# Kernel tuning notes

Hardware: AMD Instinct MI355X
Metric: run time of the kernel (lower is better)

## Reference

```python
import jax, jax.numpy as jnp
import numpy as np

DIM = 256
NUM_HEADS = 8
HEAD_DIM = DIM // NUM_HEADS


def setup_inputs() -> dict:
    key = jax.random.key(0)
    k_x, k_wq, k_bq, k_wp, k_bp = jax.random.split(key, 5)
    x = jax.random.normal(k_x, (4, DIM, 64, 64), dtype=jnp.float32)
    # 1x1 convs == per-pixel linear layers over channels
    w_qkv = jax.random.normal(k_wq, (3 * DIM, DIM), dtype=jnp.float32) * (DIM ** -0.5)
    b_qkv = jax.random.normal(k_bq, (3 * DIM,), dtype=jnp.float32) * 0.02
    w_proj = jax.random.normal(k_wp, (DIM, DIM), dtype=jnp.float32) * (DIM ** -0.5)
    b_proj = jax.random.normal(k_bp, (DIM,), dtype=jnp.float32) * 0.02
    return {"x": x, "w_qkv": w_qkv, "b_qkv": b_qkv, "w_proj": w_proj, "b_proj": b_proj}


def reference(x, w_qkv, b_qkv, w_proj, b_proj):
    B, C, H, W = x.shape
    S = H * W
    h, d = NUM_HEADS, HEAD_DIM
    # flatten spatial dims: (B, C, H, W) -> (B, S, C)
    xf = x.reshape(B, C, S).transpose(0, 2, 1)
    # 1x1 conv qkv: (B, S, 3C)
    qkv = xf @ w_qkv.T + b_qkv
    q, k, v = jnp.split(qkv, 3, axis=-1)
    # channel dim splits as (heads, head_dim): (B, S, C) -> (B, h, S, d)
    split = lambda t: t.reshape(B, S, h, d).transpose(0, 2, 1, 3)
    q, k, v = split(q), split(k), split(v)
    scale = d ** -0.5
    attn = jnp.einsum('bhsd,bhtd->bhst', q, k) * scale  # (B, h, S, S)
    attn = jax.nn.softmax(attn, axis=-1)
    out = jnp.einsum('bhst,bhtd->bhsd', attn, v)
    # merge heads: (B, h, S, d) -> (B, S, C)
    out = out.transpose(0, 2, 1, 3).reshape(B, S, C)
    out = out @ w_proj.T + b_proj
    # back to (B, C, H, W)
    return out.transpose(0, 2, 1).reshape(B, C, H, W)
```

## Files before the change

### kernel.cpp

```cpp
#include <hip/hip_runtime.h>


typedef __attribute__((ext_vector_type(8))) short short8;
typedef __attribute__((ext_vector_type(4))) float f4;

__device__ __forceinline__ short f2bs(float f) {
  union { float f; unsigned u; } v; v.f = f;
  unsigned r = v.u + 0x7FFFu + ((v.u >> 16) & 1u);
  return (short)(r >> 16);
}

__device__ __forceinline__ int pkrne(float a, float b) {
  return (int)((unsigned short)f2bs(a) | ((unsigned)f2bs(b) << 16));
}

__device__ __forceinline__ int pkhu(float lo, float hi) {
  union { float f; unsigned u; } a, b; a.f = lo; b.f = hi;
  return (int)__builtin_amdgcn_perm(b.u + 0x8000u, a.u + 0x8000u, 0x07060302u);
}

__global__ __launch_bounds__(256) void k_prep_w(
    const float* __restrict__ wq, const float* __restrict__ wp,
    short* __restrict__ wqb, short* __restrict__ wpb) {
  const int i = blockIdx.x * 256 + threadIdx.x;
  const int NQ = 768 * 256 / 4;
  f4 v; short* dst; int off;
  if (i < NQ) { v = ((const f4*)wq)[i]; dst = wqb; off = i * 4; }
  else        { v = ((const f4*)wp)[i - NQ]; dst = wpb; off = (i - NQ) * 4; }
  int2 pr; pr.x = pkrne(v[0], v[1]); pr.y = pkrne(v[2], v[3]);
  *(int2*)(dst + off) = pr;
}

__global__ __launch_bounds__(256) void k_prep_x(
    const float* __restrict__ x, short* __restrict__ xT) {
  const int t = threadIdx.x;
  const int b = blockIdx.z, c0 = blockIdx.y * 64, s0 = blockIdx.x * 64;
  __shared__ __align__(16) short tile[64 * 64];
#pragma unroll
  for (int pass = 0; pass < 4; ++pass) {
    const int cl = pass * 16 + (t >> 4);
    const int sl = (t & 15) * 4;
    f4 v = *(const f4*)(x + ((size_t)(b * 256 + c0 + cl)) * 4096 + s0 + sl);
#pragma unroll
    for (int k = 0; k < 4; ++k) {
      const int s = sl + k;
      tile[s * 64 + (cl ^ ((s & 7) << 3))] = f2bs(v[k]);
    }
  }
  __syncthreads();
#pragma unroll
  for (int i = 0; i < 2; ++i) {
    const int s = t >> 2;
    const int gc = (t & 3) + i * 4;
    const int gg = gc ^ (s & 7);
    short8 row = *(const short8*)(tile + s * 64 + gg * 8);
    *(short8*)(xT + ((size_t)(b * 4096 + s0 + s)) * 256 + c0 + gc * 8) = row;
  }
}

__global__ __launch_bounds__(256) void k_qkv(
    const short* __restrict__ xT, const short* __restrict__ wqb,
    const float* __restrict__ bias,
    short* __restrict__ Qr, short* __restrict__ Kq, short* __restrict__ Vt) {
  const int tid = threadIdx.x;
  const int L = tid & 63, wv = tid >> 6;
  const int ln15 = L & 15, quad = L >> 4;
  const int mt = blockIdx.x;
  const int b = mt >> 6;
  const int s0 = (mt & 63) << 6;
  const int j0 = blockIdx.y << 6;
  const int jw = j0 + wv * 16;

  __shared__ __align__(16) short tl[4][1024];

  f4 acc[4] = {{0,0,0,0},{0,0,0,0},{0,0,0,0},{0,0,0,0}};
  const short* wb = wqb + (jw + ln15) * 256 + quad * 8;
  const short* xb = xT + (size_t)(b * 4096 + s0 + ln15) * 256 + quad * 8;

#pragma unroll
  for (int cb = 0; cb < 256; cb += 32) {
    short8 af = *(const short8*)(wb + cb);
#pragma unroll
    for (int sub = 0; sub < 4; ++sub) {
      short8 bfr = *(const short8*)(xb + sub * (16 * 256) + cb);
      acc[sub] = __builtin_amdgcn_mfma_f32_16x16x32_bf16(af, bfr, acc[sub], 0, 0, 0);
    }
  }
  float bj[4];
#pragma unroll
  for (int r = 0; r < 4; ++r) bj[r] = bias[jw + quad * 4 + r];

  const int type = j0 >> 8;
  const int hj = jw & 255;
  const int bh = b * 8 + (hj >> 5);
  const int db = hj & 31;

  if (type != 2) {
    const float qsc = 0.17677669529663689f * 1.44269504088896f;
    const float mul = (type == 0) ? qsc : 1.0f;
    short* dst = (type == 0) ? Qr : Kq;
#pragma unroll
    for (int sub = 0; sub < 4; ++sub) {
      float v0 = (acc[sub][0] + bj[0]) * mul;
      float v1 = (acc[sub][1] + bj[1]) * mul;
      float v2 = (acc[sub][2] + bj[2]) * mul;
      float v3 = (acc[sub][3] + bj[3]) * mul;
      int2 pr; pr.x = pkhu(v0, v1); pr.y = pkhu(v2, v3);
      *(int2*)(dst + (size_t)(bh * 4096 + s0 + sub * 16 + ln15) * 32 + db + quad * 4) = pr;
    }
  } else {
    short* tv = tl[wv];
#pragma unroll
    for (int sub = 0; sub < 4; ++sub) {
      const int s = sub * 16 + ln15;
#pragma unroll
      for (int r = 0; r < 4; ++r) {
        const int dl = quad * 4 + r;
        tv[dl * 64 + ((((s >> 3) ^ dl) & 7) << 3) + (s & 7)] = f2bs(acc[sub][r] + bj[r]);
      }
    }
#pragma unroll
    for (int i = 0; i < 2; ++i) {
      const int dl = i * 8 + (L >> 3);
      const int gs = L & 7;
      const int gg = gs ^ (dl & 7);
      short8 row = *(const short8*)(tv + dl * 64 + gg * 8);
      *(short8*)(Vt + (size_t)(bh * 32 + db + dl) * 4096 + s0 + gs * 8) = row;
    }
  }
}

__global__ __launch_bounds__(256, 6) void k_attn(
    const short* __restrict__ Qr, const short* __restrict__ Kq,
    const short* __restrict__ Vt, short* __restrict__ O) {
  const int tid = threadIdx.x;
  const int L = tid & 63, wv = tid >> 6;
  const int ln15 = L & 15, quad = L >> 4;
  const int bh = blockIdx.y;
  const int b = bh >> 3, h = bh & 7;
  const int qt = wv & 1, half = wv >> 1;
  const int qb = blockIdx.x * 64 + qt * 32;

  const short* Qb = Qr + (size_t)bh * 4096 * 32;
  const short* Kb = Kq + (size_t)bh * 4096 * 32 + half * 2048 * 32;
  const short* Vb = Vt + (size_t)bh * 32 * 4096 + half * 2048;

  __shared__ __align__(16) short plds[4][2048];
  __shared__ float l_up[2][32];
  short* pw = plds[wv];
  const int sw = ln15 & 14;

  short8 qf[2];
#pragma unroll
  for (int qs = 0; qs < 2; ++qs)
    qf[qs] = *(const short8*)(Qb + (qb + qs * 16 + ln15) * 32 + quad * 8);

  f4 acc[2][2] = {{{0,0,0,0},{0,0,0,0}},{{0,0,0,0},{0,0,0,0}}};
  float lsum[2] = {0.f, 0.f};
  const f4 z4 = {0.f, 0.f, 0.f, 0.f};

  const short* kp = Kb + ln15 * 32 + quad * 8;
  const short* vp = Vb + ln15 * 4096 + quad * 8;

  for (int kb = 0; kb < 2048; kb += 64) {
#pragma unroll
    for (int t = 0; t < 4; ++t) {
      short8 kf = *(const short8*)(kp + (kb + t * 16) * 32);
#pragma unroll
      for (int qs = 0; qs < 2; ++qs) {
        f4 sc = __builtin_amdgcn_mfma_f32_16x16x32_bf16(kf, qf[qs], z4, 0, 0, 0);
        float p0 = __builtin_amdgcn_exp2f(sc[0]);
        float p1 = __builtin_amdgcn_exp2f(sc[1]);
        float p2 = __builtin_amdgcn_exp2f(sc[2]);
        float p3 = __builtin_amdgcn_exp2f(sc[3]);
        lsum[qs] += (p0 + p1) + (p2 + p3);
        int2 pr;
        pr.x = pkhu(p0, p1);
        pr.y = pkhu(p2, p3);
        const int gw = ((t << 2) + quad) ^ sw;
        *(int2*)(pw + qs * 1024 + ln15 * 64 + gw * 4) = pr;
      }
    }
#pragma unroll
    for (int ks = 0; ks < 2; ++ks) {
      short8 vf0 = *(const short8*)(vp + kb + ks * 32);
      short8 vf1 = *(const short8*)(vp + 16 * 4096 + kb + ks * 32);
#pragma unroll
      for (int qs = 0; qs < 2; ++qs) {
        const int g0 = ((ks << 3) + (quad << 1)) ^ sw;
        short8 pf = *(const short8*)(pw + qs * 1024 + ln15 * 64 + g0 * 4);
        acc[qs][0] = __builtin_amdgcn_mfma_f32_16x16x32_bf16(pf, vf0, acc[qs][0], 0, 0, 0);
        acc[qs][1] = __builtin_amdgcn_mfma_f32_16x16x32_bf16(pf, vf1, acc[qs][1], 0, 0, 0);
      }
    }
  }

  float lfull[2];
#pragma unroll
  for (int qs = 0; qs < 2; ++qs) {
    float l = lsum[qs];
    l += __shfl_xor(l, 16);
    l += __shfl_xor(l, 32);
    lfull[qs] = l;
  }

  if (half == 1) {
    float* cw = (float*)plds[wv];
#pragma unroll
    for (int qs = 0; qs < 2; ++qs) {
#pragma unroll
      for (int dg = 0; dg < 2; ++dg)
#pragma unroll
        for (int r = 0; r < 4; ++r)
          cw[(qs * 16 + quad * 4 + r) * 32 + dg * 16 + ln15] = acc[qs][dg][r];
      if (quad == 0) l_up[qt][qs * 16 + ln15] = lfull[qs];
    }
  }
  __syncthreads();
  if (half == 0) {
    const float* cu = (const float*)plds[wv + 2];
#pragma unroll
    for (int qs = 0; qs < 2; ++qs) {
#pragma unroll
      for (int r = 0; r < 4; ++r) {
        const float lown = __shfl(lfull[qs], quad * 4 + r);
        const float lup = l_up[qt][qs * 16 + quad * 4 + r];
        const float rl = 1.0f / (lown + lup);
        const int sg = qb + qs * 16 + quad * 4 + r;
        short* op = O + (size_t)(b * 4096 + sg) * 256 + h * 32 + ln15;
        const int ci = (qs * 16 + quad * 4 + r) * 32 + ln15;
        op[0]  = f2bs((acc[qs][0][r] + cu[ci]) * rl);
        op[16] = f2bs((acc[qs][1][r] + cu[ci + 16]) * rl);
      }
    }
  }
}

__global__ __launch_bounds__(256) void k_proj(
    const short* __restrict__ O, const short* __restrict__ wpb,
    const float* __restrict__ bias, float* __restrict__ out) {
  const int tid = threadIdx.x;
  const int L = tid & 63, wv = tid >> 6;
  const int ln15 = L & 15, quad = L >> 4;
  const int m0 = blockIdx.x * 64 + wv * 16;
  const int n0 = blockIdx.y << 6;
  const int b = m0 >> 12, s0 = m0 & 4095;

  f4 acc[4] = {{0,0,0,0},{0,0,0,0},{0,0,0,0},{0,0,0,0}};
  const short* Ob = O + (size_t)(m0 + ln15) * 256 + quad * 8;
  const short* wb = wpb + (n0 + ln15) * 256 + quad * 8;

#pragma unroll
  for (int cb = 0; cb < 256; cb += 32) {
    short8 af = *(const short8*)(Ob + cb);
#pragma unroll
    for (int sub = 0; sub < 4; ++sub) {
      short8 bfr = *(const short8*)(wb + sub * (16 * 256) + cb);
      acc[sub] = __builtin_amdgcn_mfma_f32_16x16x32_bf16(af, bfr, acc[sub], 0, 0, 0);
    }
  }
#pragma unroll
  for (int sub = 0; sub < 4; ++sub) {
    const int c = n0 + sub * 16 + ln15;
    const float bv = bias[c];
    f4 v;
#pragma unroll
    for (int r = 0; r < 4; ++r) v[r] = acc[sub][r] + bv;
    *(f4*)(out + (size_t)b * (256 * 4096) + (size_t)c * 4096 + s0 + quad * 4) = v;
  }
}

extern "C" void kernel_launch(void* const* d_in, const int* in_sizes, int n_in,
                              void* d_out, int out_size, void* d_ws, size_t ws_size,
                              hipStream_t stream) {
  const float* x      = (const float*)d_in[0];
  const float* w_qkv  = (const float*)d_in[1];
  const float* b_qkv  = (const float*)d_in[2];
  const float* w_proj = (const float*)d_in[3];
  const float* b_proj = (const float*)d_in[4];
  float* out = (float*)d_out;

  const size_t SEG = (size_t)4 * 8 * 4096 * 32;
  short* Qr  = (short*)d_ws;
  short* Kq  = Qr + SEG;
  short* Vt  = Kq + SEG;
  short* OX  = Vt + SEG;
  short* wqb = OX + SEG;
  short* wpb = wqb + 768 * 256;

  k_prep_w<<<256, 256, 0, stream>>>(w_qkv, w_proj, wqb, wpb);
  k_prep_x<<<dim3(64, 4, 4), 256, 0, stream>>>(x, OX);
  k_qkv <<<dim3(256, 12), 256, 0, stream>>>(OX, wqb, b_qkv, Qr, Kq, Vt);
  k_attn<<<dim3(64, 32),  256, 0, stream>>>(Qr, Kq, Vt, OX);
  k_proj<<<dim3(256, 4),  256, 0, stream>>>(OX, wpb, b_proj, out);
}
```

Baseline: 366.3 us.

## Switch attention to 32x32x16 MFMA with register-resident P and permuted V layout

Rewrites the attention inner loop around 32x32x16 bf16 MFMAs. The score accumulator layout now matches the B-operand layout of the PV product, so exponentiated probabilities are packed straight into registers and no longer round-trip through LDS. The QKV kernel writes V in a permuted column order so each lane's V fragment lines up with that register layout. The intent is to drop the per-tile LDS writes and reads of P and to issue fewer, larger MFMAs. In exchange, the 16-float accumulators raise register pressure, and the occupancy hint in launch bounds is removed.

```diff
diff --git a/kernel.cpp b/kernel.cpp
--- a/kernel.cpp
+++ b/kernel.cpp
@@ -3,6 +3,7 @@
 
 typedef __attribute__((ext_vector_type(8))) short short8;
 typedef __attribute__((ext_vector_type(4))) float f4;
+typedef __attribute__((ext_vector_type(16))) float f16v;
 
 __device__ __forceinline__ short f2bs(float f) {
   union { float f; unsigned u; } v; v.f = f;
@@ -17,6 +18,11 @@
 __device__ __forceinline__ int pkhu(float lo, float hi) {
   union { float f; unsigned u; } a, b; a.f = lo; b.f = hi;
   return (int)__builtin_amdgcn_perm(b.u + 0x8000u, a.u + 0x8000u, 0x07060302u);
+}
+
+__device__ __forceinline__ short8 mk8(int a, int b, int c, int d) {
+  int4 t; t.x = a; t.y = b; t.z = c; t.w = d;
+  short8 r; __builtin_memcpy(&r, &t, 16); return r;
 }
 
 __global__ __launch_bounds__(256) void k_prep_w(
@@ -61,7 +67,7 @@
 __global__ __launch_bounds__(256) void k_qkv(
     const short* __restrict__ xT, const short* __restrict__ wqb,
     const float* __restrict__ bias,
-    short* __restrict__ Qr, short* __restrict__ Kq, short* __restrict__ Vt) {
+    short* __restrict__ Qr, short* __restrict__ Kq, short* __restrict__ Vp) {
   const int tid = threadIdx.x;
   const int L = tid & 63, wv = tid >> 6;
   const int ln15 = L & 15, quad = L >> 4;
@@ -125,113 +131,103 @@
       const int gs = L & 7;
       const int gg = gs ^ (dl & 7);
       short8 row = *(const short8*)(tv + dl * 64 + gg * 8);
-      *(short8*)(Vt + (size_t)(bh * 32 + db + dl) * 4096 + s0 + gs * 8) = row;
-    }
-  }
-}
-
-__global__ __launch_bounds__(256, 6) void k_attn(
+      union { short8 s; int4 i4; } u; u.s = row;
+      short* vrow = Vp + (size_t)(bh * 32 + db + dl) * 4096 + s0 + (gs >> 1) * 16;
+      const int o0 = (gs & 1) ? 4 : 0;
+      const int o1 = (gs & 1) ? 12 : 8;
+      int2 lo; lo.x = u.i4.x; lo.y = u.i4.y;
+      int2 hi; hi.x = u.i4.z; hi.y = u.i4.w;
+      *(int2*)(vrow + o0) = lo;
+      *(int2*)(vrow + o1) = hi;
+    }
+  }
+}
+
+__global__ __launch_bounds__(256) void k_attn(
     const short* __restrict__ Qr, const short* __restrict__ Kq,
-    const short* __restrict__ Vt, short* __restrict__ O) {
+    const short* __restrict__ Vp, short* __restrict__ O) {
   const int tid = threadIdx.x;
   const int L = tid & 63, wv = tid >> 6;
-  const int ln15 = L & 15, quad = L >> 4;
+  const int l31 = L & 31, lh = L >> 5;
   const int bh = blockIdx.y;
-  const int b = bh >> 3, h = bh & 7;
+  const int b = bh >> 3, hd = bh & 7;
   const int qt = wv & 1, half = wv >> 1;
   const int qb = blockIdx.x * 64 + qt * 32;
 
   const short* Qb = Qr + (size_t)bh * 4096 * 32;
-  const short* Kb = Kq + (size_t)bh * 4096 * 32 + half * 2048 * 32;
-  const short* Vb = Vt + (size_t)bh * 32 * 4096 + half * 2048;
-
-  __shared__ __align__(16) short plds[4][2048];
+  const short* Kb = Kq + (size_t)bh * 4096 * 32 + half * (2048 * 32);
+  const short* Vb = Vp + (size_t)bh * 32 * 4096 + half * 2048;
+
+  __shared__ float cmb[2][32 * 32];
   __shared__ float l_up[2][32];
-  short* pw = plds[wv];
-  const int sw = ln15 & 14;
-
-  short8 qf[2];
-#pragma unroll
-  for (int qs = 0; qs < 2; ++qs)
-    qf[qs] = *(const short8*)(Qb + (qb + qs * 16 + ln15) * 32 + quad * 8);
-
-  f4 acc[2][2] = {{{0,0,0,0},{0,0,0,0}},{{0,0,0,0},{0,0,0,0}}};
-  float lsum[2] = {0.f, 0.f};
-  const f4 z4 = {0.f, 0.f, 0.f, 0.f};
-
-  const short* kp = Kb + ln15 * 32 + quad * 8;
-  const short* vp = Vb + ln15 * 4096 + quad * 8;
-
-  for (int kb = 0; kb < 2048; kb += 64) {
-#pragma unroll
-    for (int t = 0; t < 4; ++t) {
-      short8 kf = *(const short8*)(kp + (kb + t * 16) * 32);
-#pragma unroll
-      for (int qs = 0; qs < 2; ++qs) {
-        f4 sc = __builtin_amdgcn_mfma_f32_16x16x32_bf16(kf, qf[qs], z4, 0, 0, 0);
-        float p0 = __builtin_amdgcn_exp2f(sc[0]);
-        float p1 = __builtin_amdgcn_exp2f(sc[1]);
-        float p2 = __builtin_amdgcn_exp2f(sc[2]);
-        float p3 = __builtin_amdgcn_exp2f(sc[3]);
-        lsum[qs] += (p0 + p1) + (p2 + p3);
-        int2 pr;
-        pr.x = pkhu(p0, p1);
-        pr.y = pkhu(p2, p3);
-        const int gw = ((t << 2) + quad) ^ sw;
-        *(int2*)(pw + qs * 1024 + ln15 * 64 + gw * 4) = pr;
-      }
-    }
-#pragma unroll
-    for (int ks = 0; ks < 2; ++ks) {
-      short8 vf0 = *(const short8*)(vp + kb + ks * 32);
-      short8 vf1 = *(const short8*)(vp + 16 * 4096 + kb + ks * 32);
-#pragma unroll
-      for (int qs = 0; qs < 2; ++qs) {
-        const int g0 = ((ks << 3) + (quad << 1)) ^ sw;
-        short8 pf = *(const short8*)(pw + qs * 1024 + ln15 * 64 + g0 * 4);
-        acc[qs][0] = __builtin_amdgcn_mfma_f32_16x16x32_bf16(pf, vf0, acc[qs][0], 0, 0, 0);
-        acc[qs][1] = __builtin_amdgcn_mfma_f32_16x16x32_bf16(pf, vf1, acc[qs][1], 0, 0, 0);
-      }
-    }
-  }
-
-  float lfull[2];
-#pragma unroll
-  for (int qs = 0; qs < 2; ++qs) {
-    float l = lsum[qs];
-    l += __shfl_xor(l, 16);
-    l += __shfl_xor(l, 32);
-    lfull[qs] = l;
-  }
+
+  short8 qf0 = *(const short8*)(Qb + (qb + l31) * 32 + 8 * lh);
+  short8 qf1 = *(const short8*)(Qb + (qb + l31) * 32 + 16 + 8 * lh);
+
+  f16v acc = {0,0,0,0,0,0,0,0,0,0,0,0,0,0,0,0};
+  const f16v z16 = {0,0,0,0,0,0,0,0,0,0,0,0,0,0,0,0};
+  float lsum = 0.f;
+
+  const short* kp = Kb + l31 * 32 + 8 * lh;
+  const short* vpp = Vb + (size_t)l31 * 4096 + 8 * lh;
+
+#pragma unroll 2
+  for (int kb = 0; kb < 2048; kb += 32) {
+    short8 kf0 = *(const short8*)(kp + kb * 32);
+    short8 kf1 = *(const short8*)(kp + kb * 32 + 16);
+    short8 vf0 = *(const short8*)(vpp + kb);
+    short8 vf1 = *(const short8*)(vpp + kb + 16);
+    f16v sc = __builtin_amdgcn_mfma_f32_32x32x16_bf16(kf0, qf0, z16, 0, 0, 0);
+    sc = __builtin_amdgcn_mfma_f32_32x32x16_bf16(kf1, qf1, sc, 0, 0, 0);
+    float p0  = __builtin_amdgcn_exp2f(sc[0]);
+    float p1  = __builtin_amdgcn_exp2f(sc[1]);
+    float p2  = __builtin_amdgcn_exp2f(sc[2]);
+    float p3  = __builtin_amdgcn_exp2f(sc[3]);
+    float p4  = __builtin_amdgcn_exp2f(sc[4]);
+    float p5  = __builtin_amdgcn_exp2f(sc[5]);
+    float p6  = __builtin_amdgcn_exp2f(sc[6]);
+    float p7  = __builtin_amdgcn_exp2f(sc[7]);
+    float p8  = __builtin_amdgcn_exp2f(sc[8]);
+    float p9  = __builtin_amdgcn_exp2f(sc[9]);
+    float p10 = __builtin_amdgcn_exp2f(sc[10]);
+    float p11 = __builtin_amdgcn_exp2f(sc[11]);
+    float p12 = __builtin_amdgcn_exp2f(sc[12]);
+    float p13 = __builtin_amdgcn_exp2f(sc[13]);
+    float p14 = __builtin_amdgcn_exp2f(sc[14]);
+    float p15 = __builtin_amdgcn_exp2f(sc[15]);
+    lsum += (((p0 + p1) + (p2 + p3)) + ((p4 + p5) + (p6 + p7))) +
+            (((p8 + p9) + (p10 + p11)) + ((p12 + p13) + (p14 + p15)));
+    short8 pb0 = mk8(pkhu(p0, p1), pkhu(p2, p3), pkhu(p4, p5), pkhu(p6, p7));
+    short8 pb1 = mk8(pkhu(p8, p9), pkhu(p10, p11), pkhu(p12, p13), pkhu(p14, p15));
+    acc = __builtin_amdgcn_mfma_f32_32x32x16_bf16(vf0, pb0, acc, 0, 0, 0);
+    acc = __builtin_amdgcn_mfma_f32_32x32x16_bf16(vf1, pb1, acc, 0, 0, 0);
+  }
+
+  const float lf = lsum + __shfl_xor(lsum, 32);
 
   if (half == 1) {
-    float* cw = (float*)plds[wv];
-#pragma unroll
-    for (int qs = 0; qs < 2; ++qs) {
-#pragma unroll
-      for (int dg = 0; dg < 2; ++dg)
-#pragma unroll
-        for (int r = 0; r < 4; ++r)
-          cw[(qs * 16 + quad * 4 + r) * 32 + dg * 16 + ln15] = acc[qs][dg][r];
-      if (quad == 0) l_up[qt][qs * 16 + ln15] = lfull[qs];
-    }
+    float* cw = cmb[qt];
+#pragma unroll
+    for (int r = 0; r < 16; ++r) {
+      const int d = (r & 3) + 8 * (r >> 2) + 4 * lh;
+      cw[l31 * 32 + (d ^ l31)] = acc[r];
+    }
+    if (lh == 0) l_up[qt][l31] = lf;
   }
   __syncthreads();
   if (half == 0) {
-    const float* cu = (const float*)plds[wv + 2];
-#pragma unroll
-    for (int qs = 0; qs < 2; ++qs) {
-#pragma unroll
-      for (int r = 0; r < 4; ++r) {
-        const float lown = __shfl(lfull[qs], quad * 4 + r);
-        const float lup = l_up[qt][qs * 16 + quad * 4 + r];
-        const float rl = 1.0f / (lown + lup);
-        const int sg = qb + qs * 16 + quad * 4 + r;
-        short* op = O + (size_t)(b * 4096 + sg) * 256 + h * 32 + ln15;
-        const int ci = (qs * 16 + quad * 4 + r) * 32 + ln15;
-        op[0]  = f2bs((acc[qs][0][r] + cu[ci]) * rl);
-        op[16] = f2bs((acc[qs][1][r] + cu[ci + 16]) * rl);
-      }
+    const float* cu = cmb[qt];
+    const float rl = 1.0f / (lf + l_up[qt][l31]);
+    short* op = O + (size_t)(b * 4096 + qb + l31) * 256 + hd * 32;
+#pragma unroll
+    for (int g = 0; g < 4; ++g) {
+      const int d0 = 4 * lh + 8 * g;
+      const float o0 = (acc[4 * g + 0] + cu[l31 * 32 + ((d0 + 0) ^ l31)]) * rl;
+      const float o1 = (acc[4 * g + 1] + cu[l31 * 32 + ((d0 + 1) ^ l31)]) * rl;
+      const float o2 = (acc[4 * g + 2] + cu[l31 * 32 + ((d0 + 2) ^ l31)]) * rl;
+      const float o3 = (acc[4 * g + 3] + cu[l31 * 32 + ((d0 + 3) ^ l31)]) * rl;
+      int2 st; st.x = pkrne(o0, o1); st.y = pkrne(o2, o3);
+      *(int2*)(op + d0) = st;
     }
   }
 }
@@ -283,14 +279,14 @@
   const size_t SEG = (size_t)4 * 8 * 4096 * 32;
   short* Qr  = (short*)d_ws;
   short* Kq  = Qr + SEG;
-  short* Vt  = Kq + SEG;
-  short* OX  = Vt + SEG;
+  short* Vp  = Kq + SEG;
+  short* OX  = Vp + SEG;
   short* wqb = OX + SEG;
   short* wpb = wqb + 768 * 256;
 
   k_prep_w<<<256, 256, 0, stream>>>(w_qkv, w_proj, wqb, wpb);
   k_prep_x<<<dim3(64, 4, 4), 256, 0, stream>>>(x, OX);
-  k_qkv <<<dim3(256, 12), 256, 0, stream>>>(OX, wqb, b_qkv, Qr, Kq, Vt);
-  k_attn<<<dim3(64, 32),  256, 0, stream>>>(Qr, Kq, Vt, OX);
+  k_qkv <<<dim3(256, 12), 256, 0, stream>>>(OX, wqb, b_qkv, Qr, Kq, Vp);
+  k_attn<<<dim3(64, 32),  256, 0, stream>>>(Qr, Kq, Vp, OX);
   k_proj<<<dim3(256, 4),  256, 0, stream>>>(OX, wpb, b_proj, out);
 }
```

Result: faster. 332.5 us (-9.2%).
